# Optimization experiments

Hardware: AMD Instinct MI355X
Metric: run time of the kernel (lower is better)

## Reference

```python
import jax, jax.numpy as jnp
import numpy as np

B, IN_DIM, K, D = 8192, 1024, 2048, 256
TAU = 1.0
BN_EPS = 1e-5


def setup_inputs() -> dict:
    key = jax.random.key(0)
    ks = jax.random.split(key, 4)
    x = jax.random.normal(ks[0], (B, IN_DIM), dtype=jnp.float32)
    u = jax.random.uniform(ks[1], (B, K), dtype=jnp.float32)  # uniform for gumbel noise
    W = jax.random.normal(ks[2], (IN_DIM, D), dtype=jnp.float32) * 0.02
    b = jnp.zeros((D,), dtype=jnp.float32)
    gamma = jnp.ones((D,), dtype=jnp.float32)
    beta = jnp.zeros((D,), dtype=jnp.float32)
    E = jax.random.normal(ks[3], (K, D), dtype=jnp.float32)  # nn.Embedding default N(0,1)
    return {"x": x, "u": u, "W": W, "b": b, "gamma": gamma, "beta": beta, "E": E}


def reference(x, u, W, b, gamma, beta, E):
    # classifier + BatchNorm1d (training mode: batch stats, biased variance)
    h = x @ W + b                                   # [B, D]
    mu = jnp.mean(h, axis=0)
    var = jnp.var(h, axis=0)
    h = (h - mu) * jax.lax.rsqrt(var + BN_EPS) * gamma + beta
    # negative squared euclidean distance via ||h||^2 - 2 h.E^T + ||e||^2 (GEMM form,
    # avoids materializing [B, K, D])
    h2 = jnp.sum(h * h, axis=-1, keepdims=True)     # [B, 1]
    e2 = jnp.sum(E * E, axis=-1)                    # [K]
    logits = -(h2 - 2.0 * (h @ E.T) + e2)           # [B, K]
    # gumbel-softmax (soft) with tau
    g = -jnp.log(-jnp.log(u + 1e-10) + 1e-10)
    assignments = jax.nn.softmax((logits + g) / TAU, axis=-1)  # [B, K]
    z = assignments @ E                             # [B, D]
    probs = jax.nn.softmax(logits, axis=-1)
    return probs, z
```

## Files before the change

kernel.cpp:

```cpp
#include <hip/hip_runtime.h>
#include <math.h>

#define B_SZ 8192
#define IN_DIM 1024
#define K_CB 2048
#define D_SZ 256
#define BN_EPS 1e-5f

typedef _Float16 f16;
typedef _Float16 f16x8 __attribute__((ext_vector_type(8)));
typedef _Float16 f16x4 __attribute__((ext_vector_type(4)));
typedef float    f32x4 __attribute__((ext_vector_type(4)));

#define GLOAD_LDS16(g, l) __builtin_amdgcn_global_load_lds(                      \
    (const __attribute__((address_space(1))) unsigned int*)(g),                  \
    (__attribute__((address_space(3))) unsigned int*)(l), 16, 0, 0)

template<int BM, int BN, int BK, int EPI, bool A32>
__global__ __launch_bounds__(256) void gemm_mfma(
    const void* __restrict__ Aptr, int lda,
    const f16* __restrict__ Bptr, int ldb,
    void* __restrict__ Cptr, int ldc, int Kdim,
    const float* __restrict__ bias)
{
    constexpr int G    = BK / 8;
    constexpr int MASK = G - 1;
    constexpr int WM = BM / 2, WN = BN / 2;
    constexpr int FM = WM / 16, FN = WN / 16;
    constexpr int CH_A = BM * G;
    constexpr int CH_B = BN * G;

    __shared__ char lds[(BM + BN) * BK * 2];
    char* As = lds;
    char* Bs = lds + BM * BK * 2;

    const int tid  = threadIdx.x;
    const int w    = tid >> 6, lane = tid & 63;
    const int wm   = w >> 1,   wn   = w & 1;
    const int row0 = blockIdx.x * BM;
    const int col0 = blockIdx.y * BN;

    f32x4 acc[FM][FN] = {};

    for (int k0 = 0; k0 < Kdim; k0 += BK) {
        #pragma unroll
        for (int i = 0; i < CH_B / 256; ++i) {
            const int base = (i * 4 + w) * 64;
            const int s = base + lane;
            const int r = s / G, c = s % G;
            const f16* src = Bptr + (size_t)(col0 + r) * ldb + k0 + ((c ^ (r & MASK)) * 8);
            GLOAD_LDS16(src, Bs + base * 16);
        }
        if (!A32) {
            #pragma unroll
            for (int i = 0; i < CH_A / 256; ++i) {
                const int base = (i * 4 + w) * 64;
                const int s = base + lane;
                const int r = s / G, c = s % G;
                const f16* src = (const f16*)Aptr + (size_t)(row0 + r) * lda + k0 + ((c ^ (r & MASK)) * 8);
                GLOAD_LDS16(src, As + base * 16);
            }
        } else {
            #pragma unroll
            for (int i = 0; i < CH_A / 256; ++i) {
                const int s = i * 256 + tid;
                const int r = s / G, c = s % G;
                const float* src = (const float*)Aptr + (size_t)(row0 + r) * lda + k0 + c * 8;
                const float4 v0 = ((const float4*)src)[0];
                const float4 v1 = ((const float4*)src)[1];
                f16x8 d;
                d[0] = (f16)v0.x; d[1] = (f16)v0.y; d[2] = (f16)v0.z; d[3] = (f16)v0.w;
                d[4] = (f16)v1.x; d[5] = (f16)v1.y; d[6] = (f16)v1.z; d[7] = (f16)v1.w;
                *(f16x8*)(As + (r * G + (c ^ (r & MASK))) * 16) = d;
            }
        }
        __syncthreads();

        #pragma unroll
        for (int kk = 0; kk < BK / 32; ++kk) {
            f16x8 af[FM], bf[FN];
            #pragma unroll
            for (int m = 0; m < FM; ++m) {
                const int r = wm * WM + m * 16 + (lane & 15);
                const int g = (kk * 4 + (lane >> 4)) ^ (r & MASK);
                af[m] = *(const f16x8*)(As + r * (BK * 2) + g * 16);
            }
            #pragma unroll
            for (int n = 0; n < FN; ++n) {
                const int r = wn * WN + n * 16 + (lane & 15);
                const int g = (kk * 4 + (lane >> 4)) ^ (r & MASK);
                bf[n] = *(const f16x8*)(Bs + r * (BK * 2) + g * 16);
            }
            #pragma unroll
            for (int m = 0; m < FM; ++m)
                #pragma unroll
                for (int n = 0; n < FN; ++n)
                    acc[m][n] = __builtin_amdgcn_mfma_f32_16x16x32_f16(af[m], bf[n], acc[m][n], 0, 0, 0);
        }
        __syncthreads();
    }

    #pragma unroll
    for (int m = 0; m < FM; ++m) {
        const int rbase = row0 + wm * WM + m * 16 + (lane >> 4) * 4;
        #pragma unroll
        for (int n = 0; n < FN; ++n) {
            const int c = col0 + wn * WN + n * 16 + (lane & 15);
            #pragma unroll
            for (int j = 0; j < 4; ++j) {
                const float v = acc[m][n][j];
                if (EPI == 0) {
                    ((float*)Cptr)[(size_t)(rbase + j) * ldc + c] = v;
                } else {
                    ((f16*)Cptr)[(size_t)(rbase + j) * ldc + c] = (f16)(v + bias[c]);
                }
            }
        }
    }
}

#define LP1 2056

__global__ __launch_bounds__(1024, 1) void fused_sm(
    const f16* __restrict__ h16, const f16* __restrict__ E16,
    const float* __restrict__ e2v, const float* __restrict__ u,
    const float* __restrict__ scale, const float* __restrict__ shift,
    float* __restrict__ probs, f16* __restrict__ assign16)
{
    __shared__ __align__(16) char lds_raw[32 * LP1 * 2];
    __shared__ float redA[16 * 16];
    f16* Bs0 = (f16*)lds_raw;
    f16* Bs1 = Bs0 + 128 * 256;
    f16* p1buf = (f16*)lds_raw;

    const int tid  = threadIdx.x;
    const int w    = tid >> 6, lane = tid & 63;
    const int q    = lane >> 4, r16 = lane & 15;
    const int g2   = w >> 3;
    const int wc   = w & 7;
    const int row0 = blockIdx.x * 32;
    const int rowA = row0 + g2 * 16;
    const int colL = wc * 16 + r16;

    f16x8 af[8];
    {
        const f16* hrow = h16 + (size_t)(rowA + r16) * D_SZ + q * 8;
        #pragma unroll
        for (int kk = 0; kk < 8; ++kk) {
            const f16x8 raw = *(const f16x8*)(hrow + kk * 32);
            const float4 scA = *(const float4*)(scale + kk * 32 + q * 8);
            const float4 scB = *(const float4*)(scale + kk * 32 + q * 8 + 4);
            const float4 shA = *(const float4*)(shift + kk * 32 + q * 8);
            const float4 shB = *(const float4*)(shift + kk * 32 + q * 8 + 4);
            f16x8 d;
            d[0] = (f16)fmaf((float)raw[0], scA.x, shA.x);
            d[1] = (f16)fmaf((float)raw[1], scA.y, shA.y);
            d[2] = (f16)fmaf((float)raw[2], scA.z, shA.z);
            d[3] = (f16)fmaf((float)raw[3], scA.w, shA.w);
            d[4] = (f16)fmaf((float)raw[4], scB.x, shB.x);
            d[5] = (f16)fmaf((float)raw[5], scB.y, shB.y);
            d[6] = (f16)fmaf((float)raw[6], scB.z, shB.z);
            d[7] = (f16)fmaf((float)raw[7], scB.w, shB.w);
            af[kk] = d;
        }
    }

    f32x4 acc[16];
    #pragma unroll
    for (int n = 0; n < 16; ++n) acc[n] = (f32x4){0.f, 0.f, 0.f, 0.f};

    #pragma unroll
    for (int i = 0; i < 4; ++i) {
        const int base = (i * 16 + w) * 64;
        const int s = base + lane;
        const int r = s >> 5, cgg = s & 31;
        GLOAD_LDS16(E16 + (size_t)r * D_SZ + ((cgg ^ (r & 31)) * 8), Bs0 + base * 8);
    }

    #pragma unroll
    for (int c = 0; c < 16; ++c) {
        f16* buf  = (c & 1) ? Bs1 : Bs0;
        f16* nbuf = (c & 1) ? Bs0 : Bs1;
        if (c < 15) {
            #pragma unroll
            for (int i = 0; i < 4; ++i) {
                const int base = (i * 16 + w) * 64;
                const int s = base + lane;
                const int r = s >> 5, cgg = s & 31;
                GLOAD_LDS16(E16 + (size_t)((c + 1) * 128 + r) * D_SZ + ((cgg ^ (r & 31)) * 8),
                            nbuf + base * 8);
            }
            asm volatile("s_waitcnt vmcnt(4)" ::: "memory");
        } else {
            asm volatile("s_waitcnt vmcnt(0)" ::: "memory");
        }
        __builtin_amdgcn_s_barrier();
        __builtin_amdgcn_sched_barrier(0);
        #pragma unroll
        for (int kk = 0; kk < 8; ++kk) {
            const int gb = (kk * 4 + q) ^ (colL & 31);
            const f16x8 bf = *(const f16x8*)(buf + colL * 256 + gb * 8);
            acc[c] = __builtin_amdgcn_mfma_f32_16x16x32_f16(af[kk], bf, acc[c], 0, 0, 0);
        }
        __builtin_amdgcn_sched_barrier(0);
        __builtin_amdgcn_s_barrier();
        __builtin_amdgcn_sched_barrier(0);
    }
    __syncthreads();

    float m1[4] = {-1e30f, -1e30f, -1e30f, -1e30f};
    #pragma unroll
    for (int n = 0; n < 16; ++n) {
        const float ec = e2v[n * 128 + colL];
        #pragma unroll
        for (int j = 0; j < 4; ++j)
            m1[j] = fmaxf(m1[j], 2.f * acc[n][j] - ec);
    }
    #pragma unroll
    for (int off = 1; off < 16; off <<= 1)
        #pragma unroll
        for (int j = 0; j < 4; ++j)
            m1[j] = fmaxf(m1[j], __shfl_xor(m1[j], off));
    if (r16 == 0)
        #pragma unroll
        for (int j = 0; j < 4; ++j) redA[w * 16 + q * 4 + j] = m1[j];
    __syncthreads();
    #pragma unroll
    for (int j = 0; j < 4; ++j) {
        float a = -1e30f;
        #pragma unroll
        for (int t = 0; t < 8; ++t) a = fmaxf(a, redA[(g2 * 8 + t) * 16 + q * 4 + j]);
        m1[j] = a;
    }

    #pragma unroll
    for (int n = 0; n < 16; ++n) {
        const float ec = e2v[n * 128 + colL];
        #pragma unroll
        for (int j = 0; j < 4; ++j) {
            const float lv = 2.f * acc[n][j] - ec;
            p1buf[(size_t)(g2 * 16 + q * 4 + j) * LP1 + n * 128 + colL] =
                (f16)__expf(lv - m1[j] + 10.f);
        }
    }
    __syncthreads();

    const int trow = tid >> 5;
    const int cg   = tid & 31;
    const float* urow = u + (size_t)(row0 + trow) * K_CB + cg * 4;
    const f16* prow_l = p1buf + (size_t)trow * LP1 + cg * 4;

    float s1 = 0.f, s2 = 0.f;
    f16x4 gv[16];
    #pragma unroll
    for (int n = 0; n < 16; ++n) {
        const float4 u4 = *(const float4*)(urow + n * 128);
        const f16x4 p4 = *(const f16x4*)(prow_l + n * 128);
        const float ua[4] = {u4.x, u4.y, u4.z, u4.w};
        #pragma unroll
        for (int e = 0; e < 4; ++e) {
            const f16 g = (f16)(-__logf(-__logf(ua[e] + 1e-10f) + 1e-10f));
            gv[n][e] = g;
            s1 += (float)p4[e];
            s2 += (float)p4[e] * __expf((float)g);
        }
    }
    #pragma unroll
    for (int off = 1; off < 32; off <<= 1) {
        s1 += __shfl_xor(s1, off);
        s2 += __shfl_xor(s2, off);
    }
    const float r1 = 1.f / s1;
    const float r2 = 1.f / s2;

    float* prow = probs + (size_t)(row0 + trow) * K_CB + cg * 4;
    f16* arow = assign16 + (size_t)(row0 + trow) * K_CB + cg * 4;
    #pragma unroll
    for (int n = 0; n < 16; ++n) {
        const f16x4 p4 = *(const f16x4*)(prow_l + n * 128);
        float4 o;
        o.x = (float)p4[0] * r1; o.y = (float)p4[1] * r1;
        o.z = (float)p4[2] * r1; o.w = (float)p4[3] * r1;
        *(float4*)(prow + n * 128) = o;
        f16x4 a4;
        #pragma unroll
        for (int e = 0; e < 4; ++e)
            a4[e] = (f16)((float)p4[e] * __expf((float)gv[n][e]) * r2);
        *(f16x4*)(arow + n * 128) = a4;
    }
}

template<bool DIRECT>
__global__ __launch_bounds__(256) void transp_f16(
    const float* __restrict__ src, f16* __restrict__ dstT, f16* __restrict__ dst,
    int R, int C)
{
    __shared__ f16 tile[64][66];
    const int tr = blockIdx.x * 64, tc = blockIdx.y * 64;
    const int lr = threadIdx.x >> 4;
    const int lc = (threadIdx.x & 15) * 4;

    #pragma unroll
    for (int i = 0; i < 4; ++i) {
        const int row = i * 16 + lr;
        const float4 v = *(const float4*)(src + (size_t)(tr + row) * C + tc + lc);
        f16 h0 = (f16)v.x, h1 = (f16)v.y, h2 = (f16)v.z, h3 = (f16)v.w;
        tile[row][lc + 0] = h0; tile[row][lc + 1] = h1;
        tile[row][lc + 2] = h2; tile[row][lc + 3] = h3;
        if (DIRECT) {
            f16x4 d; d[0] = h0; d[1] = h1; d[2] = h2; d[3] = h3;
            *(f16x4*)(dst + (size_t)(tr + row) * C + tc + lc) = d;
        }
    }
    __syncthreads();
    #pragma unroll
    for (int i = 0; i < 4; ++i) {
        const int drow = i * 16 + lr;
        f16x4 o;
        o[0] = tile[lc + 0][drow]; o[1] = tile[lc + 1][drow];
        o[2] = tile[lc + 2][drow]; o[3] = tile[lc + 3][drow];
        *(f16x4*)(dstT + (size_t)(tc + drow) * R + tr + lc) = o;
    }
}

__global__ __launch_bounds__(256) void e2_kernel(const float* __restrict__ E, float* __restrict__ e2)
{
    const int wave = threadIdx.x >> 6, lane = threadIdx.x & 63;
    const int row = blockIdx.x * 4 + wave;
    const float4 v = ((const float4*)(E + (size_t)row * D_SZ))[lane];
    float ss = v.x * v.x + v.y * v.y + v.z * v.z + v.w * v.w;
    #pragma unroll
    for (int off = 32; off > 0; off >>= 1) ss += __shfl_down(ss, off);
    if (lane == 0) e2[row] = ss;
}

__global__ __launch_bounds__(256) void bn_partial(const f16* __restrict__ h16, float* __restrict__ part)
{
    const int d = threadIdx.x;
    const int blk = blockIdx.x;
    const int r0 = blk * (B_SZ / 128);
    float s = 0.f, sq = 0.f;
    for (int r = r0; r < r0 + (B_SZ / 128); ++r) {
        const float v = (float)h16[(size_t)r * D_SZ + d];
        s += v; sq += v * v;
    }
    part[blk * 512 + d]       = s;
    part[blk * 512 + 256 + d] = sq;
}

__global__ __launch_bounds__(256) void bn_finalize(
    const float* __restrict__ part, const float* __restrict__ gamma, const float* __restrict__ beta,
    float* __restrict__ scale, float* __restrict__ shift)
{
    const int d = threadIdx.x;
    float s = 0.f, sq = 0.f;
    for (int b = 0; b < 128; ++b) { s += part[b * 512 + d]; sq += part[b * 512 + 256 + d]; }
    const float mu  = s / (float)B_SZ;
    const float var = sq / (float)B_SZ - mu * mu;
    const float sc  = gamma[d] * rsqrtf(var + BN_EPS);
    scale[d] = sc;
    shift[d] = beta[d] - mu * sc;
}

extern "C" void kernel_launch(void* const* d_in, const int* in_sizes, int n_in,
                              void* d_out, int out_size, void* d_ws, size_t ws_size,
                              hipStream_t stream)
{
    const float* x     = (const float*)d_in[0];
    const float* u     = (const float*)d_in[1];
    const float* W     = (const float*)d_in[2];
    const float* bias  = (const float*)d_in[3];
    const float* gamma = (const float*)d_in[4];
    const float* beta  = (const float*)d_in[5];
    const float* E     = (const float*)d_in[6];

    float* probs = (float*)d_out;
    float* z     = probs + (size_t)B_SZ * K_CB;

    char* ws = (char*)d_ws;
    f16* assign16 = (f16*)ws;  ws += (size_t)B_SZ * K_CB * 2;
    f16* h16 = (f16*)ws;       ws += (size_t)B_SZ * D_SZ * 2;
    f16* WT16 = (f16*)ws;      ws += (size_t)D_SZ * IN_DIM * 2;
    f16* E16 = (f16*)ws;       ws += (size_t)K_CB * D_SZ * 2;
    f16* ET16 = (f16*)ws;      ws += (size_t)D_SZ * K_CB * 2;
    float* part = (float*)ws;  ws += 128 * 512 * 4;
    float* scale = (float*)ws; ws += D_SZ * 4;
    float* shift = (float*)ws; ws += D_SZ * 4;
    float* e2 = (float*)ws;    ws += K_CB * 4;

    {
        dim3 gW(IN_DIM / 64, D_SZ / 64);
        transp_f16<false><<<gW, 256, 0, stream>>>(W, WT16, nullptr, IN_DIM, D_SZ);
        dim3 gE(K_CB / 64, D_SZ / 64);
        transp_f16<true><<<gE, 256, 0, stream>>>(E, ET16, E16, K_CB, D_SZ);
    }
    e2_kernel<<<K_CB / 4, 256, 0, stream>>>(E, e2);

    {
        dim3 g(B_SZ / 64, D_SZ / 64);
        gemm_mfma<64, 64, 64, 1, true><<<g, 256, 0, stream>>>(
            x, IN_DIM, WT16, IN_DIM, h16, D_SZ, IN_DIM, bias);
    }
    bn_partial<<<128, 256, 0, stream>>>(h16, part);
    bn_finalize<<<1, 256, 0, stream>>>(part, gamma, beta, scale, shift);

    fused_sm<<<B_SZ / 32, 1024, 0, stream>>>(h16, E16, e2, u, scale, shift, probs, assign16);

    {
        dim3 g(B_SZ / 64, D_SZ / 64);
        gemm_mfma<64, 64, 128, 0, false><<<g, 256, 0, stream>>>(
            assign16, K_CB, ET16, K_CB, z, D_SZ, K_CB, nullptr);
    }
}
```

Measured before the change: 116.0 us.

## Move BN normalization to separate kernel and reload A fragments per chunk

```diff
diff --git a/kernel.cpp b/kernel.cpp
--- a/kernel.cpp
+++ b/kernel.cpp
@@ -124,7 +124,6 @@
 __global__ __launch_bounds__(1024, 1) void fused_sm(
     const f16* __restrict__ h16, const f16* __restrict__ E16,
     const float* __restrict__ e2v, const float* __restrict__ u,
-    const float* __restrict__ scale, const float* __restrict__ shift,
     float* __restrict__ probs, f16* __restrict__ assign16)
 {
     __shared__ __align__(16) char lds_raw[32 * LP1 * 2];
@@ -142,28 +141,7 @@
     const int rowA = row0 + g2 * 16;
     const int colL = wc * 16 + r16;
 
-    f16x8 af[8];
-    {
-        const f16* hrow = h16 + (size_t)(rowA + r16) * D_SZ + q * 8;
-        #pragma unroll
-        for (int kk = 0; kk < 8; ++kk) {
-            const f16x8 raw = *(const f16x8*)(hrow + kk * 32);
-            const float4 scA = *(const float4*)(scale + kk * 32 + q * 8);
-            const float4 scB = *(const float4*)(scale + kk * 32 + q * 8 + 4);
-            const float4 shA = *(const float4*)(shift + kk * 32 + q * 8);
-            const float4 shB = *(const float4*)(shift + kk * 32 + q * 8 + 4);
-            f16x8 d;
-            d[0] = (f16)fmaf((float)raw[0], scA.x, shA.x);
-            d[1] = (f16)fmaf((float)raw[1], scA.y, shA.y);
-            d[2] = (f16)fmaf((float)raw[2], scA.z, shA.z);
-            d[3] = (f16)fmaf((float)raw[3], scA.w, shA.w);
-            d[4] = (f16)fmaf((float)raw[4], scB.x, shB.x);
-            d[5] = (f16)fmaf((float)raw[5], scB.y, shB.y);
-            d[6] = (f16)fmaf((float)raw[6], scB.z, shB.z);
-            d[7] = (f16)fmaf((float)raw[7], scB.w, shB.w);
-            af[kk] = d;
-        }
-    }
+    const f16* hrow = h16 + (size_t)(rowA + r16) * D_SZ + q * 8;
 
     f32x4 acc[16];
     #pragma unroll
@@ -181,6 +159,14 @@
     for (int c = 0; c < 16; ++c) {
         f16* buf  = (c & 1) ? Bs1 : Bs0;
         f16* nbuf = (c & 1) ? Bs0 : Bs1;
+
+        int zz;
+        asm volatile("v_mov_b32 %0, 0" : "=v"(zz));
+        f16x8 af[8];
+        #pragma unroll
+        for (int kk = 0; kk < 8; ++kk)
+            af[kk] = *(const f16x8*)(hrow + kk * 32 + zz);
+
         if (c < 15) {
             #pragma unroll
             for (int i = 0; i < 4; ++i) {
@@ -360,6 +346,22 @@
     const float sc  = gamma[d] * rsqrtf(var + BN_EPS);
     scale[d] = sc;
     shift[d] = beta[d] - mu * sc;
+}
+
+__global__ __launch_bounds__(256) void norm_h(
+    f16* __restrict__ h16, const float* __restrict__ scale, const float* __restrict__ shift)
+{
+    const int wave = threadIdx.x >> 6, lane = threadIdx.x & 63;
+    const int row = blockIdx.x * 4 + wave;
+    f16x4* hp = (f16x4*)(h16 + (size_t)row * D_SZ);
+    f16x4 v = hp[lane];
+    const float4 sc = ((const float4*)scale)[lane];
+    const float4 sh = ((const float4*)shift)[lane];
+    v[0] = (f16)fmaf((float)v[0], sc.x, sh.x);
+    v[1] = (f16)fmaf((float)v[1], sc.y, sh.y);
+    v[2] = (f16)fmaf((float)v[2], sc.z, sh.z);
+    v[3] = (f16)fmaf((float)v[3], sc.w, sh.w);
+    hp[lane] = v;
 }
 
 extern "C" void kernel_launch(void* const* d_in, const int* in_sizes, int n_in,
@@ -403,8 +405,9 @@
     }
     bn_partial<<<128, 256, 0, stream>>>(h16, part);
     bn_finalize<<<1, 256, 0, stream>>>(part, gamma, beta, scale, shift);
-
-    fused_sm<<<B_SZ / 32, 1024, 0, stream>>>(h16, E16, e2, u, scale, shift, probs, assign16);
+    norm_h<<<B_SZ / 4, 256, 0, stream>>>(h16, scale, shift);
+
+    fused_sm<<<B_SZ / 32, 1024, 0, stream>>>(h16, E16, e2, u, probs, assign16);
 
     {
         dim3 g(B_SZ / 64, D_SZ / 64);
```

After: 167.1 us. 1.44x slower.
